# Performance work log

Hardware: AMD Instinct MI355X
Metric: run time of the kernel (lower is better)

Reference implementation:

```python
import jax, jax.numpy as jnp
import numpy as np

# Conv config (matches init_kwargs)
STRIDE = (1, 1)
PADDING = ((1, 1), (1, 1))
B, CIN, COUT, H, W = 16, 128, 256, 56, 56
KH, KW = 3, 3


def _conv(x, w):
    # NCHW input, OIHW kernel, zeros padding mode
    return jax.lax.conv_general_dilated(
        x, w, window_strides=STRIDE, padding=PADDING,
        dimension_numbers=("NCHW", "OIHW", "NCHW"))


def setup_inputs() -> dict:
    key = jax.random.key(0)
    ks = jax.random.split(key, 6)
    x = jax.random.normal(ks[0], (B, CIN, H, W), dtype=jnp.float32)
    # quantized weight: integer-valued floats (output of module.Q.quantize)
    weight = jnp.round(jax.random.normal(ks[1], (COUT, CIN, KH, KW), dtype=jnp.float32) * 4.0)
    act_s = jnp.asarray(0.0625, dtype=jnp.float32)   # exp2(log_act_s)
    act_q = jnp.asarray(16.0, dtype=jnp.float32)     # exp2(log_act_q)
    azp = jnp.asarray(-4.0, dtype=jnp.float32)       # rounded act zero point (scaled by guard_a)
    wzp = jnp.round(jax.random.normal(ks[2], (COUT,), dtype=jnp.float32) * 2.0)
    fp_scale = (jax.random.uniform(ks[3], (1, COUT, 1, 1), dtype=jnp.float32) + 0.5) * 1e-3
    # bias_full has spatial extent [1, COUT, H_out, W_out]
    bias = jax.random.normal(ks[4], (1, COUT, H, W), dtype=jnp.float32) * 0.1
    guard_a = jnp.asarray(2.0, dtype=jnp.float32)    # 2**act_guard_bit
    guard_w = jnp.asarray(2.0, dtype=jnp.float32)    # 2**weight_guard_bit
    return {"x": x, "weight": weight, "act_s": act_s, "act_q": act_q,
            "azp": azp, "wzp": wzp, "fp_scale": fp_scale, "bias": bias,
            "guard_a": guard_a, "guard_w": guard_w}


def reference(x, weight, act_s, act_q, azp, wzp, fp_scale, bias, guard_a, guard_w):
    # 1) Activation quantization: clamp to quant range then round to integer grid.
    zp = azp * act_s / guard_a
    xq = jnp.clip(x, zp, zp + act_q - act_s)
    xq = guard_a * jnp.round((xq - zp) / act_s)
    # 2) Main integer conv with quantized weights.
    c1 = _conv(xq, weight)
    # 3) Ones-kernel conv: output is identical across all COUT channels,
    #    so compute once as channel-sum followed by a single-channel box conv.
    s = jnp.sum(xq, axis=1, keepdims=True)  # [B, 1, H, W]
    ones_k = jnp.ones((1, 1) + weight.shape[2:], dtype=x.dtype)
    c2 = _conv(s, ones_k)  # [B, 1, H_out, W_out], broadcasts over channels
    # 4) Affine dequant + spatially-varying bias epilogue.
    out = guard_w * c1 + wzp[None, :, None, None] * c2
    return out * fp_scale + bias
```

## Files before the change

kernel.cpp:

```cpp
#include <hip/hip_runtime.h>

#define B_    16
#define CIN_  128
#define COUT_ 256
#define H_    56
#define W_    56
#define YP    58
#define XP    64

typedef int   i32x4 __attribute__((ext_vector_type(4)));
typedef float f32x4 __attribute__((ext_vector_type(4)));

#define BH_SZ 16640
#define EP_STRIDE 68

__device__ __forceinline__ void gload16(const void* g, void* l) {
    __builtin_amdgcn_global_load_lds(
        (const __attribute__((address_space(1))) unsigned int*)g,
        (__attribute__((address_space(3))) unsigned int*)l,
        16, 0, 0);
}

__global__ __launch_bounds__(256) void k_prep(
    const float* __restrict__ x, const float* __restrict__ w,
    const float* __restrict__ p_act_s, const float* __restrict__ p_act_q,
    const float* __restrict__ p_azp,  const float* __restrict__ p_guard_a,
    signed char* __restrict__ xqU, signed char* __restrict__ wt,
    float* __restrict__ s_pad, float* __restrict__ Wsum)
{
    int t = threadIdx.x;
    int blk = blockIdx.x;

    if (blk < 928) {
        int b = blk / YP, y = blk - b * YP;
        __shared__ signed char shq[W_ * 144];
        signed char* orow = xqU + (size_t)blk * XP * CIN_;

        if (y == 0 || y == YP - 1) {
            i32x4 pv = {(int)0x80808080, (int)0x80808080,
                        (int)0x80808080, (int)0x80808080};
            *(i32x4*)(orow + t * 32)      = pv;
            *(i32x4*)(orow + t * 32 + 16) = pv;
            if (t < XP) s_pad[(size_t)blk * XP + t] = 0.0f;
            return;
        }
        int h = y - 1;
        float act_s = p_act_s[0], act_q = p_act_q[0];
        float azp = p_azp[0], ga = p_guard_a[0];
        float zp = azp * act_s / ga;
        float hi = zp + act_q - act_s;
        float inv_s = 1.0f / act_s;

        for (int i = 0; i < 28; ++i) {
            int e = i * 256 + t;
            int cin = e / 56;
            int ww = e - cin * 56;
            float v = x[(((size_t)b * CIN_ + cin) * H_ + h) * W_ + ww];
            v = fminf(fmaxf(v, zp), hi);
            float r = rintf((v - zp) * inv_s);
            float uq = rintf(ga * r * 0.5f) - 128.0f;
            shq[ww * 144 + cin] = (signed char)(int)uq;
        }
        __syncthreads();
        #pragma unroll
        for (int i = 0; i < 2; ++i) {
            int T = i * 256 + t;
            int xx = T >> 3;
            int c16 = T & 7;
            union { i32x4 v; signed char c[16]; } u;
            if (xx >= 1 && xx <= W_) {
                u.v = *(const i32x4*)(shq + (xx - 1) * 144 + c16 * 16);
            } else {
                u.v = (i32x4){(int)0x80808080, (int)0x80808080,
                              (int)0x80808080, (int)0x80808080};
            }
            *(i32x4*)(orow + (size_t)xx * CIN_ + c16 * 16) = u.v;
            int sum = 0;
            #pragma unroll
            for (int j = 0; j < 16; ++j) sum += (int)u.c[j];
            sum += __shfl_xor(sum, 1);
            sum += __shfl_xor(sum, 2);
            sum += __shfl_xor(sum, 4);
            if (c16 == 0)
                s_pad[(size_t)blk * XP + xx] = (float)(2 * sum + 32768);
        }
        return;
    }

    if (blk < 1216) {
        int o = ((blk - 928) * 256 + t) * 4;
        int tile = o >> 13;
        int m    = (o >> 6) & 127;
        int kk   = o & 63;
        int cb = tile & 1, cc = (tile >> 1) & 1, g = tile >> 2;
        int cout = cb * 128 + m;
        int cin0 = cc * 64 + kk;
        int dy = g / 3, dx = g - dy * 3;
        union { int v; signed char c[4]; } pk;
        #pragma unroll
        for (int j = 0; j < 4; ++j) {
            float v = w[(size_t)cout * 1152 + (cin0 + j) * 9 + dy * 3 + dx];
            pk.c[j] = (signed char)(int)v;
        }
        *(int*)(wt + o) = pk.v;
        return;
    }

    {
        int bw = blk - 1216;
        int cout = bw * 16 + (t >> 4);
        int part = t & 15;
        const float* base = w + (size_t)cout * 1152 + part * 72;
        float s = 0.f;
        for (int j = 0; j < 72; ++j) s += base[j];
        s += __shfl_xor(s, 1);
        s += __shfl_xor(s, 2);
        s += __shfl_xor(s, 4);
        s += __shfl_xor(s, 8);
        if (part == 0) Wsum[cout] = s;
        return;
    }
}

__global__ __launch_bounds__(256, 3) void k_gemm(
    const signed char* __restrict__ xqU,
    const signed char* __restrict__ wt,
    const float* __restrict__ s_pad,
    const float* __restrict__ Wsum,
    const float* __restrict__ wzp,
    const float* __restrict__ fps,
    const float* __restrict__ bias,
    const float* __restrict__ p_gw,
    float* __restrict__ out)
{
    __shared__ union {
        signed char bh[2][BH_SZ];
        float       ep[128 * EP_STRIDE];
    } smem;
    __shared__ float c2s[2 * 56];

    int tid = threadIdx.x;
    int wv = tid >> 6, lane = tid & 63;
    int xl = lane & 15, q = lane >> 4;
    int p = blockIdx.x, cb = blockIdx.y;
    int b = p / 28, hp = p - b * 28;
    int h = hp * 2;
    int wm0 = (wv >> 1) * 64;
    int row = wv & 1;

    if (tid < 112) {
        int rr = tid / 56, wp = tid - rr * 56;
        const float* sp = s_pad + ((size_t)(b * YP + h + rr)) * XP + wp;
        float a = 0.f;
        #pragma unroll
        for (int dy = 0; dy < 3; ++dy)
            #pragma unroll
            for (int dx = 0; dx < 3; ++dx)
                a += sp[dy * XP + dx];
        c2s[tid] = a;
    }

    const signed char* xb = xqU + (size_t)(b * YP + h) * XP * CIN_;

    #define STAGE_B(buf_, cc_)                                              \
        {                                                                   \
            signed char* dstb = smem.bh[buf_];                              \
            _Pragma("unroll")                                               \
            for (int r_ = 0; r_ < 4; ++r_) {                                \
                int T_ = r_ * 256 + tid;                                    \
                int p_ = T_ & 3;                                            \
                int x_ = (T_ >> 2) & 63;                                    \
                int yy_ = T_ >> 8;                                          \
                int q_ = p_ ^ ((x_ >> 1) & 3);                              \
                gload16(xb + (size_t)(yy_ * XP + x_) * CIN_ + (cc_) * 64 + q_ * 16, \
                        dstb + (r_ * 256 + wv * 64) * 16);                  \
            }                                                               \
        }

    STAGE_B(0, 0)
    __syncthreads();

    i32x4 acc[4][4];
    #pragma unroll
    for (int mi = 0; mi < 4; ++mi)
        #pragma unroll
        for (int ni = 0; ni < 4; ++ni)
            acc[mi][ni] = (i32x4){0, 0, 0, 0};

    int aoff = (wm0 + xl) * 64 + q * 16;

    #pragma unroll
    for (int cc = 0; cc < 2; ++cc) {
        const signed char* Bb = smem.bh[cc];
        #pragma unroll
        for (int g = 0; g < 9; ++g) {
            if (cc == 0 && g == 0) STAGE_B(1, 1)
            int dy = g / 3, dx = g - dy * 3;
            const signed char* wtile =
                wt + (size_t)(((g * 2 + cc) * 2) + cb) * 8192;
            int slot = q ^ (((xl + dx) >> 1) & 3);
            int boff = (row + dy) * 4096 + (xl + dx) * 64 + slot * 16;
            i32x4 af[4], bf[4];
            #pragma unroll
            for (int mi = 0; mi < 4; ++mi)
                af[mi] = *(const i32x4*)(wtile + aoff + mi * 1024);
            #pragma unroll
            for (int ni = 0; ni < 4; ++ni)
                bf[ni] = *(const i32x4*)(Bb + boff + ni * 1024);
            #pragma unroll
            for (int mi = 0; mi < 4; ++mi)
                #pragma unroll
                for (int ni = 0; ni < 4; ++ni)
                    acc[mi][ni] = __builtin_amdgcn_mfma_i32_16x16x64_i8(
                        af[mi], bf[ni], acc[mi][ni], 0, 0, 0);
        }
        if (cc == 0) __syncthreads();
    }

    __syncthreads();

    float gw = p_gw[0];
    int cout_l = tid & 127;
    int half   = tid >> 7;
    int cout_g = cb * 128 + cout_l;
    float fs = fps[cout_g];
    float A  = gw * fs;
    float K0 = 256.0f * gw * Wsum[cout_g] * fs;
    float B0 = wzp[cout_g] * fs;

    #pragma unroll
    for (int r2 = 0; r2 < 2; ++r2) {
        if (row == r2) {
            #pragma unroll
            for (int mi = 0; mi < 4; ++mi)
                #pragma unroll
                for (int ni = 0; ni < 4; ++ni)
                    #pragma unroll
                    for (int r = 0; r < 4; ++r)
                        smem.ep[(wm0 + mi * 16 + q * 4 + r) * EP_STRIDE +
                                ni * 16 + xl] = 2.0f * (float)acc[mi][ni][r];
        }
        __syncthreads();
        {
            int hrow = h + r2;
            const float* brow = bias + ((size_t)cout_g * H_ + hrow) * W_;
            float* orow = out + (((size_t)b * COUT_ + cout_g) * H_ + hrow) * W_;
            const float* eprow = smem.ep + cout_l * EP_STRIDE;
            const float* c2row = c2s + r2 * 56;
            #pragma unroll
            for (int j = 0; j < 7; ++j) {
                int w4 = (half * 7 + j) * 4;
                f32x4 e = *(const f32x4*)(eprow + w4);
                f32x4 bi = *(const f32x4*)(brow + w4);
                f32x4 c2v = *(const f32x4*)(c2row + w4);
                f32x4 v;
                #pragma unroll
                for (int kq = 0; kq < 4; ++kq)
                    v[kq] = A * e[kq] + K0 + B0 * c2v[kq] + bi[kq];
                *(f32x4*)(orow + w4) = v;
            }
        }
        if (r2 == 0) __syncthreads();
    }
}

extern "C" void kernel_launch(void* const* d_in, const int* in_sizes, int n_in,
                              void* d_out, int out_size, void* d_ws, size_t ws_size,
                              hipStream_t stream)
{
    const float* x     = (const float*)d_in[0];
    const float* wht   = (const float*)d_in[1];
    const float* act_s = (const float*)d_in[2];
    const float* act_q = (const float*)d_in[3];
    const float* azp   = (const float*)d_in[4];
    const float* wzp   = (const float*)d_in[5];
    const float* fps   = (const float*)d_in[6];
    const float* bias  = (const float*)d_in[7];
    const float* ga    = (const float*)d_in[8];
    const float* gw    = (const float*)d_in[9];
    float* out = (float*)d_out;

    char* ws = (char*)d_ws;
    signed char* xqU  = (signed char*)(ws);
    signed char* wt   = (signed char*)(ws + 7602176);
    float*       spad = (float*)(ws + 7602176 + 294912);
    float*       Wsum = (float*)(ws + 7602176 + 294912 + 237568);

    k_prep<<<dim3(1232), dim3(256), 0, stream>>>(
        x, wht, act_s, act_q, azp, ga, xqU, wt, spad, Wsum);
    k_gemm<<<dim3(448, 2), dim3(256), 0, stream>>>(
        xqU, wt, spad, Wsum, wzp, fps, bias, gw, out);
}
```

Measured before the change: 153.7 us.

## Stage both channel halves upfront and software-pipeline weight loads across taps

Both input channel halves are now staged into shared memory before a single barrier, which removes the mid-loop barrier. The loop is restructured over the 9 filter taps with both channel chunks per iteration, and the next tap's weight fragments are prefetched from global memory into registers while the current tap's MFMAs run. This hides global weight-load latency behind compute. The extra register buffers raise register pressure, so launch bounds drop from 3 to 2 blocks per SM, which reduces occupancy.

```diff
diff --git a/kernel.cpp b/kernel.cpp
--- a/kernel.cpp
+++ b/kernel.cpp
@@ -122,7 +122,7 @@
     }
 }
 
-__global__ __launch_bounds__(256, 3) void k_gemm(
+__global__ __launch_bounds__(256, 2) void k_gemm(
     const signed char* __restrict__ xqU,
     const signed char* __restrict__ wt,
     const float* __restrict__ s_pad,
@@ -162,9 +162,9 @@
 
     const signed char* xb = xqU + (size_t)(b * YP + h) * XP * CIN_;
 
-    #define STAGE_B(buf_, cc_)                                              \
+    #define STAGE_B(cc_)                                                    \
         {                                                                   \
-            signed char* dstb = smem.bh[buf_];                              \
+            signed char* dstb = smem.bh[cc_];                               \
             _Pragma("unroll")                                               \
             for (int r_ = 0; r_ < 4; ++r_) {                                \
                 int T_ = r_ * 256 + tid;                                    \
@@ -177,8 +177,18 @@
             }                                                               \
         }
 
-    STAGE_B(0, 0)
-    __syncthreads();
+    STAGE_B(0)
+    STAGE_B(1)
+
+    int aoff = (wm0 + xl) * 64 + q * 16;
+
+    i32x4 a0[2][4];
+    #pragma unroll
+    for (int cc = 0; cc < 2; ++cc)
+        #pragma unroll
+        for (int mi = 0; mi < 4; ++mi)
+            a0[cc][mi] = *(const i32x4*)(
+                wt + (size_t)((0 * 2 + cc) * 2 + cb) * 8192 + aoff + mi * 1024);
 
     i32x4 acc[4][4];
     #pragma unroll
@@ -187,34 +197,42 @@
         for (int ni = 0; ni < 4; ++ni)
             acc[mi][ni] = (i32x4){0, 0, 0, 0};
 
-    int aoff = (wm0 + xl) * 64 + q * 16;
+    __syncthreads();
 
     #pragma unroll
-    for (int cc = 0; cc < 2; ++cc) {
-        const signed char* Bb = smem.bh[cc];
-        #pragma unroll
-        for (int g = 0; g < 9; ++g) {
-            if (cc == 0 && g == 0) STAGE_B(1, 1)
-            int dy = g / 3, dx = g - dy * 3;
-            const signed char* wtile =
-                wt + (size_t)(((g * 2 + cc) * 2) + cb) * 8192;
-            int slot = q ^ (((xl + dx) >> 1) & 3);
-            int boff = (row + dy) * 4096 + (xl + dx) * 64 + slot * 16;
-            i32x4 af[4], bf[4];
-            #pragma unroll
-            for (int mi = 0; mi < 4; ++mi)
-                af[mi] = *(const i32x4*)(wtile + aoff + mi * 1024);
+    for (int g = 0; g < 9; ++g) {
+        i32x4 an[2][4];
+        if (g < 8) {
+            #pragma unroll
+            for (int cc = 0; cc < 2; ++cc)
+                #pragma unroll
+                for (int mi = 0; mi < 4; ++mi)
+                    an[cc][mi] = *(const i32x4*)(
+                        wt + (size_t)(((g + 1) * 2 + cc) * 2 + cb) * 8192 +
+                        aoff + mi * 1024);
+        }
+        int dy = g / 3, dx = g - dy * 3;
+        int slot = q ^ (((xl + dx) >> 1) & 3);
+        int boff = (row + dy) * 4096 + (xl + dx) * 64 + slot * 16;
+        i32x4 bf[2][4];
+        #pragma unroll
+        for (int cc = 0; cc < 2; ++cc)
             #pragma unroll
             for (int ni = 0; ni < 4; ++ni)
-                bf[ni] = *(const i32x4*)(Bb + boff + ni * 1024);
+                bf[cc][ni] = *(const i32x4*)(smem.bh[cc] + boff + ni * 1024);
+        #pragma unroll
+        for (int cc = 0; cc < 2; ++cc)
             #pragma unroll
             for (int mi = 0; mi < 4; ++mi)
                 #pragma unroll
                 for (int ni = 0; ni < 4; ++ni)
                     acc[mi][ni] = __builtin_amdgcn_mfma_i32_16x16x64_i8(
-                        af[mi], bf[ni], acc[mi][ni], 0, 0, 0);
-        }
-        if (cc == 0) __syncthreads();
+                        a0[cc][mi], bf[cc][ni], acc[mi][ni], 0, 0, 0);
+        #pragma unroll
+        for (int cc = 0; cc < 2; ++cc)
+            #pragma unroll
+            for (int mi = 0; mi < 4; ++mi)
+                a0[cc][mi] = an[cc][mi];
     }
 
     __syncthreads();
```

Result: faster. 150.2 us (-2.3%).
